# Optimization experiments

Hardware: AMD Instinct MI355X
Metric: run time of the kernel (lower is better)

The kernel has to match this reference:

```python
import jax, jax.numpy as jnp
import numpy as np

B, T, H = 16, 512, 768
S = 32            # gold spans per example
L = 50            # max_span_len -> candidate ends per span
NT = 3            # num_types
HS = 4 * H        # span repr size


def setup_inputs() -> dict:
    key = jax.random.key(0)
    ks = jax.random.split(key, 8)
    h = jax.random.normal(ks[0], (B, T, H), dtype=jnp.float32)
    attention_mask = jnp.ones((B, T), dtype=jnp.int32)
    starts = jax.random.randint(ks[1], (B, S), 1, 400).astype(jnp.int32)
    lens = jax.random.randint(ks[2], (B, S), 0, L).astype(jnp.int32)
    ends = starts + lens                      # <= 448 < last_tok=510
    types = jax.random.randint(ks[3], (B, S), 0, NT).astype(jnp.int32)
    W1 = jax.random.normal(ks[4], (HS, HS), dtype=jnp.float32) * (1.0 / np.sqrt(HS))
    b1 = jnp.zeros((HS,), dtype=jnp.float32)
    w_score = jax.random.normal(ks[5], (HS,), dtype=jnp.float32) * (1.0 / np.sqrt(HS))
    b_score = jnp.zeros((1,), dtype=jnp.float32)
    W_type = jax.random.normal(ks[6], (HS, NT), dtype=jnp.float32) * (1.0 / np.sqrt(HS))
    b_type = jnp.zeros((NT,), dtype=jnp.float32)
    return {"h": h, "attention_mask": attention_mask, "span_starts": starts,
            "span_ends": ends, "span_types": types, "W1": W1, "b1": b1,
            "w_score": w_score, "b_score": b_score, "W_type": W_type, "b_type": b_type}


def _span_loss(h, attention_mask, span_starts, span_ends, span_types,
               W1, b1, w_score, b_score, W_type, b_type, type_loss_weight=1.0):
    cls = h[:, 0]                                              # [B,H]
    # prefix sums for O(1) segment means: pre[b,t] = sum h[b,0:t]
    pre = jnp.concatenate([jnp.zeros((B, 1, H), h.dtype), jnp.cumsum(h, axis=1)], axis=1)

    valid_len = attention_mask.sum(axis=1)                     # [B]
    last_tok = jnp.maximum(1, valid_len - 2)                   # [B]

    s = span_starts                                            # [B,S]
    e_gold = span_ends
    gold_idx = e_gold - s                                      # [B,S]
    lt = last_tok[:, None]
    span_valid = (s >= 1) & (s <= lt) & (e_gold >= s) & (e_gold <= lt) & (gold_idx < L)

    e_max = jnp.minimum(s + L - 1, lt)                         # [B,S]
    p = s[..., None] + jnp.arange(L, dtype=s.dtype)            # [B,S,L] candidate ends
    cand_valid = p <= e_max[..., None]

    sc = jnp.clip(s, 0, T - 1)
    pc = jnp.clip(p, 0, T - 1)
    bi2 = jnp.arange(B)[:, None]
    bi3 = jnp.arange(B)[:, None, None]

    h_start = h[bi2, sc]                                       # [B,S,H]
    h_end = h[bi3, pc]                                         # [B,S,L,H]
    seg_len = jnp.maximum(p - s[..., None] + 1, 1).astype(h.dtype)
    h_mean = (pre[bi3, pc + 1] - pre[bi2, sc][:, :, None]) / seg_len[..., None]

    repr_ = jnp.concatenate([
        jnp.broadcast_to(h_start[:, :, None], (B, S, L, H)),
        h_end,
        h_mean,
        jnp.broadcast_to(cls[:, None, None], (B, S, L, H)),
    ], axis=-1)                                                # [B,S,L,4H]

    h1 = jax.nn.gelu(jnp.einsum('bslh,hd->bsld', repr_, W1) + b1, approximate=False)
    scores = jnp.einsum('bsld,d->bsl', h1, w_score) + b_score[0]      # [B,S,L]
    type_logits = jnp.einsum('bsld,dk->bslk', h1, W_type) + b_type    # [B,S,L,NT]

    # end-index CE over valid candidate ends
    masked = jnp.where(cand_valid, scores, jnp.float32(-1e9))
    logp_end = jax.nn.log_softmax(masked, axis=-1)             # [B,S,L]
    gi = jnp.clip(gold_idx, 0, L - 1)
    end_loss = -jnp.take_along_axis(logp_end, gi[..., None], axis=-1)[..., 0]  # [B,S]

    # type CE at the gold end index
    tl_gold = jnp.take_along_axis(type_logits, gi[..., None, None], axis=2)[:, :, 0]  # [B,S,NT]
    logp_t = jax.nn.log_softmax(tl_gold, axis=-1)
    tg = jnp.clip(span_types, 0, NT - 1)
    type_loss = -jnp.take_along_axis(logp_t, tg[..., None], axis=-1)[..., 0]  # [B,S]

    vmask = span_valid.astype(h.dtype)
    n_seg = vmask.sum()
    denom = jnp.maximum(n_seg, 1.0)
    loss_end = jnp.where(n_seg > 0, (end_loss * vmask).sum() / denom, 0.0)
    loss_type = jnp.where(n_seg > 0, (type_loss * vmask).sum() / denom, 0.0)
    return loss_end + type_loss_weight * loss_type


def reference(h, attention_mask, span_starts, span_ends, span_types,
              W1, b1, w_score, b_score, W_type, b_type):
    return _span_loss(h, attention_mask, span_starts, span_ends, span_types,
                      W1, b1, w_score, b_score, W_type, b_type)
```

## Files before the change

kernel.cpp:

```cpp
#include <hip/hip_runtime.h>
#include <hip/hip_bf16.h>
#include <math.h>

#define B_ 16
#define T_ 512
#define H_ 768
#define S_ 32
#define L_ 50
#define NT_ 3
#define HS_ 3072
#define CH_ 8
#define CT_ 64

#define XROWS 8192
#define YBASE 8192
#define GBASE 16512
#define XYROWS 16400
#define AROWS 17152

typedef __attribute__((ext_vector_type(8))) short short8;
typedef __attribute__((ext_vector_type(4))) float float4v;

__device__ __forceinline__ float bf2f(unsigned short u) {
    union { unsigned int i; float f; } v; v.i = ((unsigned int)u) << 16; return v.f;
}
__device__ __forceinline__ void load_lds16(const void* g, void* l) {
    __builtin_amdgcn_global_load_lds((__attribute__((address_space(1))) void*)g,
                                     (__attribute__((address_space(3))) void*)l, 16, 0, 0);
}

__device__ __forceinline__ float gelu_exact(float v) {
    float a = fabsf(v) * 0.70710678118654752f;
    float t = __builtin_amdgcn_rcpf(fmaf(a, 0.47047f, 1.0f));
    float poly = t * fmaf(t, fmaf(t, 0.7478556f, -0.0958798f), 0.3480242f);
    float e = __builtin_amdgcn_exp2f(a * a * -1.4426950408889634f);
    float erfa = fmaf(-poly, e, 1.0f);
    float erfv = copysignf(erfa, v);
    return 0.5f * v * (1.0f + erfv);
}

__global__ __launch_bounds__(256) void cumsum_pass1(const float* __restrict__ h,
                                                    float* __restrict__ partial) {
    int idx = blockIdx.x * 256 + threadIdx.x;
    int hd = idx % H_; int t = idx / H_; int ch = t % CH_; int b = t / CH_;
    const float* hp = h + ((size_t)b * T_ + ch * CT_) * H_ + hd;
    float acc = 0.f;
#pragma unroll 8
    for (int tt = 0; tt < CT_; tt++) acc += hp[(size_t)tt * H_];
    partial[idx] = acc;
}

__global__ __launch_bounds__(256) void cumsum_pass2(float* __restrict__ partial) {
    int idx = blockIdx.x * 256 + threadIdx.x;
    int hd = idx % H_, b = idx / H_;
    float acc = 0.f;
#pragma unroll
    for (int ch = 0; ch < CH_; ch++) {
        size_t o = ((size_t)b * CH_ + ch) * H_ + hd;
        float v = partial[o];
        partial[o] = acc;
        acc += v;
    }
}

__global__ __launch_bounds__(256) void cumsum_pass3(const float* __restrict__ h,
                                                    const float* __restrict__ partial,
                                                    __hip_bfloat16* __restrict__ Ab) {
    int idx = blockIdx.x * 256 + threadIdx.x;
    int hd = idx % H_; int t = idx / H_; int ch = t % CH_; int b = t / CH_;
    float acc = partial[idx];
    int row0 = b * T_ + ch * CT_;
    const float* hp = h + (size_t)row0 * H_ + hd;
    __hip_bfloat16* hb = Ab + (size_t)row0 * H_ + hd;
    __hip_bfloat16* pp = Ab + ((size_t)(YBASE + b * (T_ + 1) + ch * CT_ + 1)) * H_ + hd;
    if (ch == 0) Ab[((size_t)(YBASE + b * (T_ + 1))) * H_ + hd] = __float2bfloat16(0.f);
#pragma unroll 8
    for (int tt = 0; tt < CT_; tt++) {
        float hv = hp[(size_t)tt * H_];
        hb[(size_t)tt * H_] = __float2bfloat16(hv);
        acc += hv;
        pp[(size_t)tt * H_] = __float2bfloat16(acc);
    }
}

__global__ void gather_kernel(const float* __restrict__ h,
                              const int* __restrict__ starts,
                              __hip_bfloat16* __restrict__ Ab) {
    int r = blockIdx.x;
    int src_row;
    if (r < B_ * S_) {
        int b = r / S_;
        int sv = starts[r];
        int sc = min(max(sv, 0), T_ - 1);
        src_row = b * T_ + sc;
    } else {
        int b = r - B_ * S_;
        src_row = b * T_;
    }
    __hip_bfloat16* dst = Ab + (size_t)(GBASE + r) * H_;
    for (int j = threadIdx.x; j < H_; j += 256)
        dst[j] = __float2bfloat16(h[(size_t)src_row * H_ + j]);
}

__global__ __launch_bounds__(256) void transpose_w(const float* __restrict__ W1,
                                                   __hip_bfloat16* __restrict__ Wt) {
    __shared__ float tile[64][65];
    int n0 = blockIdx.x * 64, k0 = blockIdx.y * 64;
    int c = threadIdx.x & 63, r0 = threadIdx.x >> 6;
#pragma unroll
    for (int i = 0; i < 16; i++) {
        int r = r0 + i * 4;
        tile[r][c] = W1[(size_t)(k0 + r) * HS_ + n0 + c];
    }
    __syncthreads();
    int p = k0 / H_, kl = k0 % H_;
    __hip_bfloat16* out = Wt + (size_t)p * HS_ * H_;
#pragma unroll
    for (int i = 0; i < 16; i++) {
        int r = r0 + i * 4;
        out[(size_t)(n0 + r) * H_ + kl + c] = __float2bfloat16(tile[c][r]);
    }
}

__global__ __launch_bounds__(256) void mfma_gemm(const __hip_bfloat16* __restrict__ Ab,
                                                 const __hip_bfloat16* __restrict__ Wt,
                                                 __hip_bfloat16* __restrict__ XY,
                                                 float* __restrict__ ST,
                                                 float* __restrict__ CC) {
    constexpr int K = H_;
    __shared__ __hip_bfloat16 As[128 * 32];
    __shared__ __hip_bfloat16 Bs[128 * 32];
    int tid = threadIdx.x;
    int wave = tid >> 6, lane = tid & 63;
    int m0 = blockIdx.y * 128, n0 = blockIdx.x * 128;
    int wm = (wave & 1) * 64, wn = (wave >> 1) * 64;

    const __hip_bfloat16* Bt;
    if (m0 < XROWS)            Bt = Wt + (size_t)1 * HS_ * H_;
    else if (m0 < GBASE)       Bt = Wt + (size_t)2 * HS_ * H_;
    else if (m0 < GBASE + 512) Bt = Wt;
    else                       Bt = Wt + (size_t)3 * HS_ * H_;

    float4v acc[4][4] = {};

    int c1 = wave * 128 + lane;
    int c2 = c1 + 64;
    int lr = lane & 15, lq = lane >> 4;

    for (int k0 = 0; k0 < K; k0 += 32) {
        __syncthreads();
        load_lds16(Ab + (size_t)(m0 + (c1 >> 2)) * K + k0 + (c1 & 3) * 8,
                   &As[(size_t)(wave * 128) * 8]);
        load_lds16(Ab + (size_t)(m0 + (c2 >> 2)) * K + k0 + (c2 & 3) * 8,
                   &As[(size_t)(wave * 128 + 64) * 8]);
        load_lds16(Bt + (size_t)(n0 + (c1 >> 2)) * K + k0 + (c1 & 3) * 8,
                   &Bs[(size_t)(wave * 128) * 8]);
        load_lds16(Bt + (size_t)(n0 + (c2 >> 2)) * K + k0 + (c2 & 3) * 8,
                   &Bs[(size_t)(wave * 128 + 64) * 8]);
        __syncthreads();

        short8 af[4], bf[4];
        const short* Asp = (const short*)As;
        const short* Bsp = (const short*)Bs;
#pragma unroll
        for (int mi = 0; mi < 4; mi++)
            af[mi] = *(const short8*)&Asp[(wm + mi * 16 + lr) * 32 + lq * 8];
#pragma unroll
        for (int ni = 0; ni < 4; ni++)
            bf[ni] = *(const short8*)&Bsp[(wn + ni * 16 + lr) * 32 + lq * 8];
#pragma unroll
        for (int mi = 0; mi < 4; mi++)
#pragma unroll
            for (int ni = 0; ni < 4; ni++)
                acc[mi][ni] = __builtin_amdgcn_mfma_f32_16x16x32_bf16(
                    af[mi], bf[ni], acc[mi][ni], 0, 0, 0);
    }

    int col = lane & 15, rq = (lane >> 4) * 4;
#pragma unroll
    for (int mi = 0; mi < 4; mi++) {
#pragma unroll
        for (int ni = 0; ni < 4; ni++) {
#pragma unroll
            for (int r = 0; r < 4; r++) {
                int m = m0 + wm + mi * 16 + rq + r;
                int n = n0 + wn + ni * 16 + col;
                float v = acc[mi][ni][r];
                if (m < XYROWS) {
                    XY[(size_t)m * HS_ + n] = __float2bfloat16(v);
                } else if (m >= GBASE && m < GBASE + 512) {
                    ST[(size_t)(m - GBASE) * HS_ + n] = v;
                } else if (m >= GBASE + 512 && m < GBASE + 528) {
                    CC[(size_t)(m - GBASE - 512) * HS_ + n] = v;
                }
            }
        }
    }
}

__global__ __launch_bounds__(256) void c0_kernel(float4* __restrict__ ST,
                                                 const float4* __restrict__ CC,
                                                 const float4* __restrict__ b1) {
    int i = blockIdx.x * 256 + threadIdx.x;
    int row = i / (HS_ / 4);
    int b = row >> 5;
    int c4 = i % (HS_ / 4);
    float4 s = ST[i], c = CC[b * (HS_ / 4) + c4], bb = b1[c4];
    s.x += c.x + bb.x; s.y += c.y + bb.y; s.z += c.z + bb.z; s.w += c.w + bb.w;
    ST[i] = s;
}

__global__ __launch_bounds__(256) void combine_kernel(
    const float* __restrict__ c0, const __hip_bfloat16* __restrict__ XY,
    const float* __restrict__ w_score, const float* __restrict__ b_score,
    const float* __restrict__ W_type,
    const int* __restrict__ starts, const int* __restrict__ ends,
    float* __restrict__ scores, float* __restrict__ tgold) {
    int bs = blockIdx.x;
    int b = bs >> 5;
    int wave = threadIdx.x >> 6, lane = threadIdx.x & 63;
    int l = blockIdx.y * 4 + wave;
    if (l >= L_) return;
    int sv = starts[bs], ev = ends[bs];
    int gi = min(max(ev - sv, 0), L_ - 1);
    int sc = min(max(sv, 0), T_ - 1);
    int p = sv + l;
    int pc = min(max(p, 0), T_ - 1);
    float invlen = 1.0f / (float)(l + 1);
    bool isg = (l == gi);

    const unsigned short* Xr = (const unsigned short*)(XY + (size_t)(b * T_ + pc) * HS_);
    const unsigned short* Yp = (const unsigned short*)(XY + (size_t)(YBASE + b * (T_ + 1) + pc + 1) * HS_);
    const unsigned short* Ys = (const unsigned short*)(XY + (size_t)(YBASE + b * (T_ + 1) + sc) * HS_);
    const float* c0r = c0 + (size_t)bs * HS_;

    float local = 0.f, t0 = 0.f, t1 = 0.f, t2 = 0.f;
#pragma unroll
    for (int j = 0; j < 6; j++) {
        int d = j * 512 + lane * 8;
        short8 xv = *(const short8*)(Xr + d);
        short8 yv = *(const short8*)(Yp + d);
        short8 sv8 = *(const short8*)(Ys + d);
        float4 ca = *(const float4*)(c0r + d);
        float4 cb = *(const float4*)(c0r + d + 4);
        float4 wa = *(const float4*)(w_score + d);
        float4 wb = *(const float4*)(w_score + d + 4);
        float cv[8] = {ca.x, ca.y, ca.z, ca.w, cb.x, cb.y, cb.z, cb.w};
        float wv[8] = {wa.x, wa.y, wa.z, wa.w, wb.x, wb.y, wb.z, wb.w};
#pragma unroll
        for (int q = 0; q < 8; q++) {
            float x = bf2f(((const unsigned short*)&xv)[q]);
            float y = bf2f(((const unsigned short*)&yv)[q]);
            float ys = bf2f(((const unsigned short*)&sv8)[q]);
            float v = fmaf(y - ys, invlen, cv[q]) + x;
            float g = gelu_exact(v);
            local = fmaf(g, wv[q], local);
            if (isg) {
                t0 = fmaf(g, W_type[(d + q) * NT_ + 0], t0);
                t1 = fmaf(g, W_type[(d + q) * NT_ + 1], t1);
                t2 = fmaf(g, W_type[(d + q) * NT_ + 2], t2);
            }
        }
    }
#pragma unroll
    for (int off = 32; off >= 1; off >>= 1) local += __shfl_down(local, off);
    if (lane == 0) scores[(size_t)bs * L_ + l] = local + b_score[0];
    if (isg) {
#pragma unroll
        for (int off = 32; off >= 1; off >>= 1) {
            t0 += __shfl_down(t0, off);
            t1 += __shfl_down(t1, off);
            t2 += __shfl_down(t2, off);
        }
        if (lane == 0) {
            tgold[bs * NT_ + 0] = t0;
            tgold[bs * NT_ + 1] = t1;
            tgold[bs * NT_ + 2] = t2;
        }
    }
}

__global__ __launch_bounds__(512) void loss_kernel(
    const float* __restrict__ scores, const float* __restrict__ tgold,
    const int* __restrict__ mask, const int* __restrict__ starts,
    const int* __restrict__ ends, const int* __restrict__ types,
    const float* __restrict__ b_type, float* __restrict__ out) {
    __shared__ int svl[B_];
    __shared__ float r[3][8];
    int tid = threadIdx.x;
    int b = tid / S_;
    if (tid < B_) svl[tid] = 0;
    __syncthreads();
    {
        int part = 0;
        const int* mp = mask + tid * 16;
#pragma unroll
        for (int i = 0; i < 16; i++) part += mp[i];
        atomicAdd(&svl[tid / (T_ / 16)], part);
    }
    __syncthreads();
    int vl = svl[b];
    int lt = max(1, vl - 2);
    int sv = starts[tid], ev = ends[tid];
    int gold = ev - sv;
    bool valid = (sv >= 1) && (sv <= lt) && (ev >= sv) && (ev <= lt) && (gold < L_);
    int emax = min(sv + L_ - 1, lt);
    const float* sp = scores + (size_t)tid * L_;
    float m = -1e30f;
    for (int l = 0; l < L_; l++) {
        float v = (sv + l <= emax) ? sp[l] : -1e9f;
        m = fmaxf(m, v);
    }
    float sum = 0.f;
    for (int l = 0; l < L_; l++) {
        float v = (sv + l <= emax) ? sp[l] : -1e9f;
        sum += expf(v - m);
    }
    int gi = min(max(gold, 0), L_ - 1);
    float vg = (sv + gi <= emax) ? sp[gi] : -1e9f;
    float end_loss = (m + logf(sum)) - vg;

    float t0 = tgold[tid * 3 + 0] + b_type[0];
    float t1 = tgold[tid * 3 + 1] + b_type[1];
    float t2 = tgold[tid * 3 + 2] + b_type[2];
    float tm = fmaxf(t0, fmaxf(t1, t2));
    float tsum = expf(t0 - tm) + expf(t1 - tm) + expf(t2 - tm);
    int tg = min(max(types[tid], 0), NT_ - 1);
    float tv = (tg == 0) ? t0 : ((tg == 1) ? t1 : t2);
    float type_loss = (tm + logf(tsum)) - tv;

    float ve = valid ? end_loss : 0.f;
    float vt = valid ? type_loss : 0.f;
    float vc = valid ? 1.f : 0.f;
    for (int off = 32; off >= 1; off >>= 1) {
        ve += __shfl_down(ve, off);
        vt += __shfl_down(vt, off);
        vc += __shfl_down(vc, off);
    }
    if ((tid & 63) == 0) {
        int w = tid >> 6;
        r[0][w] = ve; r[1][w] = vt; r[2][w] = vc;
    }
    __syncthreads();
    if (tid == 0) {
        float se = 0, st = 0, n = 0;
        for (int w = 0; w < 8; w++) { se += r[0][w]; st += r[1][w]; n += r[2][w]; }
        float denom = fmaxf(n, 1.f);
        out[0] = (n > 0.f) ? (se / denom + st / denom) : 0.f;
    }
}

extern "C" void kernel_launch(void* const* d_in, const int* in_sizes, int n_in,
                              void* d_out, int out_size, void* d_ws, size_t ws_size,
                              hipStream_t stream) {
    const float* h       = (const float*)d_in[0];
    const int*   mask    = (const int*)d_in[1];
    const int*   starts  = (const int*)d_in[2];
    const int*   ends    = (const int*)d_in[3];
    const int*   types   = (const int*)d_in[4];
    const float* W1      = (const float*)d_in[5];
    const float* b1      = (const float*)d_in[6];
    const float* w_score = (const float*)d_in[7];
    const float* b_score = (const float*)d_in[8];
    const float* W_type  = (const float*)d_in[9];
    const float* b_type  = (const float*)d_in[10];
    float* out = (float*)d_out;

    char* ws = (char*)d_ws;
    size_t off = 0;
    __hip_bfloat16* Ab = (__hip_bfloat16*)(ws + off); off += (size_t)AROWS * H_ * 2;
    __hip_bfloat16* XY = (__hip_bfloat16*)(ws + off); off += (size_t)XYROWS * HS_ * 2;
    __hip_bfloat16* Wt = (__hip_bfloat16*)(ws + off); off += (size_t)4 * HS_ * H_ * 2;
    float* ST     = (float*)(ws + off);               off += (size_t)512 * HS_ * 4;
    float* CC     = (float*)(ws + off);               off += (size_t)16 * HS_ * 4;
    float* scores = (float*)(ws + off);               off += (size_t)B_ * S_ * L_ * 4;
    float* tgold  = (float*)(ws + off);               off += (size_t)B_ * S_ * NT_ * 4;
    float* partial = (float*)XY;

    hipLaunchKernelGGL(cumsum_pass1, dim3(B_ * CH_ * H_ / 256), dim3(256), 0, stream, h, partial);
    hipLaunchKernelGGL(cumsum_pass2, dim3(B_ * H_ / 256), dim3(256), 0, stream, partial);
    hipLaunchKernelGGL(cumsum_pass3, dim3(B_ * CH_ * H_ / 256), dim3(256), 0, stream, h, partial, Ab);
    hipLaunchKernelGGL(gather_kernel, dim3(B_ * S_ + B_), dim3(256), 0, stream, h, starts, Ab);
    hipLaunchKernelGGL(transpose_w, dim3(48, 48), dim3(256), 0, stream, W1, Wt);

    hipLaunchKernelGGL(mfma_gemm, dim3(24, AROWS / 128), dim3(256), 0, stream,
                       Ab, Wt, XY, ST, CC);
    hipLaunchKernelGGL(c0_kernel, dim3(512 * HS_ / 4 / 256), dim3(256), 0, stream,
                       (float4*)ST, (const float4*)CC, (const float4*)b1);
    hipLaunchKernelGGL(combine_kernel, dim3(B_ * S_, 13), dim3(256), 0, stream,
                       ST, XY, w_score, b_score, W_type, starts, ends, scores, tgold);
    hipLaunchKernelGGL(loss_kernel, dim3(1), dim3(512), 0, stream,
                       scores, tgold, mask, starts, ends, types, b_type, out);
}
```

Before: 376.0 us.

## Switch GEMM to 32x32 MFMA with K=64 steps, fuse scan pass, bf16 c0

```diff
diff --git a/kernel.cpp b/kernel.cpp
--- a/kernel.cpp
+++ b/kernel.cpp
@@ -19,8 +19,12 @@
 #define AROWS 17152
 
 typedef __attribute__((ext_vector_type(8))) short short8;
-typedef __attribute__((ext_vector_type(4))) float float4v;
-
+typedef __attribute__((ext_vector_type(16))) float float16v;
+
+__device__ __forceinline__ unsigned short f2bf(float f) {
+    __hip_bfloat16 b = __float2bfloat16(f);
+    return *(unsigned short*)&b;
+}
 __device__ __forceinline__ float bf2f(unsigned short u) {
     union { unsigned int i; float f; } v; v.i = ((unsigned int)u) << 16; return v.f;
 }
@@ -50,25 +54,15 @@
     partial[idx] = acc;
 }
 
-__global__ __launch_bounds__(256) void cumsum_pass2(float* __restrict__ partial) {
-    int idx = blockIdx.x * 256 + threadIdx.x;
-    int hd = idx % H_, b = idx / H_;
-    float acc = 0.f;
-#pragma unroll
-    for (int ch = 0; ch < CH_; ch++) {
-        size_t o = ((size_t)b * CH_ + ch) * H_ + hd;
-        float v = partial[o];
-        partial[o] = acc;
-        acc += v;
-    }
-}
-
 __global__ __launch_bounds__(256) void cumsum_pass3(const float* __restrict__ h,
                                                     const float* __restrict__ partial,
                                                     __hip_bfloat16* __restrict__ Ab) {
     int idx = blockIdx.x * 256 + threadIdx.x;
     int hd = idx % H_; int t = idx / H_; int ch = t % CH_; int b = t / CH_;
-    float acc = partial[idx];
+    float acc = 0.f;
+#pragma unroll
+    for (int c = 0; c < CH_; c++)
+        if (c < ch) acc += partial[((size_t)b * CH_ + c) * H_ + hd];
     int row0 = b * T_ + ch * CT_;
     const float* hp = h + (size_t)row0 * H_ + hd;
     __hip_bfloat16* hb = Ab + (size_t)row0 * H_ + hd;
@@ -128,11 +122,11 @@
                                                  float* __restrict__ ST,
                                                  float* __restrict__ CC) {
     constexpr int K = H_;
-    __shared__ __hip_bfloat16 As[128 * 32];
-    __shared__ __hip_bfloat16 Bs[128 * 32];
+    __shared__ __hip_bfloat16 As[2][128][32];
+    __shared__ __hip_bfloat16 Bs[2][128][32];
     int tid = threadIdx.x;
     int wave = tid >> 6, lane = tid & 63;
-    int m0 = blockIdx.y * 128, n0 = blockIdx.x * 128;
+    int m0 = blockIdx.x * 128, n0 = blockIdx.y * 128;
     int wm = (wave & 1) * 64, wn = (wave >> 1) * 64;
 
     const __hip_bfloat16* Bt;
@@ -141,50 +135,54 @@
     else if (m0 < GBASE + 512) Bt = Wt;
     else                       Bt = Wt + (size_t)3 * HS_ * H_;
 
-    float4v acc[4][4] = {};
-
-    int c1 = wave * 128 + lane;
-    int c2 = c1 + 64;
-    int lr = lane & 15, lq = lane >> 4;
-
-    for (int k0 = 0; k0 < K; k0 += 32) {
+    float16v acc[2][2] = {};
+
+    int l31 = lane & 31, lh = lane >> 5;
+
+    for (int k0 = 0; k0 < K; k0 += 64) {
         __syncthreads();
-        load_lds16(Ab + (size_t)(m0 + (c1 >> 2)) * K + k0 + (c1 & 3) * 8,
-                   &As[(size_t)(wave * 128) * 8]);
-        load_lds16(Ab + (size_t)(m0 + (c2 >> 2)) * K + k0 + (c2 & 3) * 8,
-                   &As[(size_t)(wave * 128 + 64) * 8]);
-        load_lds16(Bt + (size_t)(n0 + (c1 >> 2)) * K + k0 + (c1 & 3) * 8,
-                   &Bs[(size_t)(wave * 128) * 8]);
-        load_lds16(Bt + (size_t)(n0 + (c2 >> 2)) * K + k0 + (c2 & 3) * 8,
-                   &Bs[(size_t)(wave * 128 + 64) * 8]);
+#pragma unroll
+        for (int i = 0; i < 4; i++) {
+            int c = i * 256 + wave * 64 + lane;
+            int hh = c >> 9, row = (c >> 2) & 127, kc = c & 3;
+            size_t go = (size_t)row * K + k0 + hh * 32 + kc * 8;
+            char* ldsbase = (char*)As + (size_t)(i * 256 + wave * 64) * 16;
+            load_lds16(Ab + (size_t)m0 * K + go, ldsbase);
+            char* ldsbaseB = (char*)Bs + (size_t)(i * 256 + wave * 64) * 16;
+            load_lds16(Bt + (size_t)n0 * K + go, ldsbaseB);
+        }
         __syncthreads();
 
-        short8 af[4], bf[4];
         const short* Asp = (const short*)As;
         const short* Bsp = (const short*)Bs;
 #pragma unroll
-        for (int mi = 0; mi < 4; mi++)
-            af[mi] = *(const short8*)&Asp[(wm + mi * 16 + lr) * 32 + lq * 8];
-#pragma unroll
-        for (int ni = 0; ni < 4; ni++)
-            bf[ni] = *(const short8*)&Bsp[(wn + ni * 16 + lr) * 32 + lq * 8];
-#pragma unroll
-        for (int mi = 0; mi < 4; mi++)
-#pragma unroll
-            for (int ni = 0; ni < 4; ni++)
-                acc[mi][ni] = __builtin_amdgcn_mfma_f32_16x16x32_bf16(
-                    af[mi], bf[ni], acc[mi][ni], 0, 0, 0);
-    }
-
-    int col = lane & 15, rq = (lane >> 4) * 4;
-#pragma unroll
-    for (int mi = 0; mi < 4; mi++) {
-#pragma unroll
-        for (int ni = 0; ni < 4; ni++) {
-#pragma unroll
-            for (int r = 0; r < 4; r++) {
-                int m = m0 + wm + mi * 16 + rq + r;
-                int n = n0 + wn + ni * 16 + col;
+        for (int kk = 0; kk < 4; kk++) {
+            int hh = kk >> 1;
+            int ko = (kk & 1) * 16 + lh * 8;
+            short8 af[2], bf[2];
+#pragma unroll
+            for (int mi = 0; mi < 2; mi++)
+                af[mi] = *(const short8*)&Asp[hh * 4096 + (wm + mi * 32 + l31) * 32 + ko];
+#pragma unroll
+            for (int ni = 0; ni < 2; ni++)
+                bf[ni] = *(const short8*)&Bsp[hh * 4096 + (wn + ni * 32 + l31) * 32 + ko];
+#pragma unroll
+            for (int mi = 0; mi < 2; mi++)
+#pragma unroll
+                for (int ni = 0; ni < 2; ni++)
+                    acc[mi][ni] = __builtin_amdgcn_mfma_f32_32x32x16_bf16(
+                        af[mi], bf[ni], acc[mi][ni], 0, 0, 0);
+        }
+    }
+
+#pragma unroll
+    for (int mi = 0; mi < 2; mi++) {
+#pragma unroll
+        for (int ni = 0; ni < 2; ni++) {
+            int n = n0 + wn + ni * 32 + l31;
+#pragma unroll
+            for (int r = 0; r < 16; r++) {
+                int m = m0 + wm + mi * 32 + (r & 3) + 8 * (r >> 2) + 4 * lh;
                 float v = acc[mi][ni][r];
                 if (m < XYROWS) {
                     XY[(size_t)m * HS_ + n] = __float2bfloat16(v);
@@ -198,20 +196,25 @@
     }
 }
 
-__global__ __launch_bounds__(256) void c0_kernel(float4* __restrict__ ST,
+__global__ __launch_bounds__(256) void c0_kernel(const float4* __restrict__ ST,
                                                  const float4* __restrict__ CC,
-                                                 const float4* __restrict__ b1) {
+                                                 const float4* __restrict__ b1,
+                                                 ushort4* __restrict__ c0b) {
     int i = blockIdx.x * 256 + threadIdx.x;
     int row = i / (HS_ / 4);
     int b = row >> 5;
     int c4 = i % (HS_ / 4);
     float4 s = ST[i], c = CC[b * (HS_ / 4) + c4], bb = b1[c4];
-    s.x += c.x + bb.x; s.y += c.y + bb.y; s.z += c.z + bb.z; s.w += c.w + bb.w;
-    ST[i] = s;
+    ushort4 o;
+    o.x = f2bf(s.x + c.x + bb.x);
+    o.y = f2bf(s.y + c.y + bb.y);
+    o.z = f2bf(s.z + c.z + bb.z);
+    o.w = f2bf(s.w + c.w + bb.w);
+    c0b[i] = o;
 }
 
 __global__ __launch_bounds__(256) void combine_kernel(
-    const float* __restrict__ c0, const __hip_bfloat16* __restrict__ XY,
+    const unsigned short* __restrict__ c0, const __hip_bfloat16* __restrict__ XY,
     const float* __restrict__ w_score, const float* __restrict__ b_score,
     const float* __restrict__ W_type,
     const int* __restrict__ starts, const int* __restrict__ ends,
@@ -232,7 +235,7 @@
     const unsigned short* Xr = (const unsigned short*)(XY + (size_t)(b * T_ + pc) * HS_);
     const unsigned short* Yp = (const unsigned short*)(XY + (size_t)(YBASE + b * (T_ + 1) + pc + 1) * HS_);
     const unsigned short* Ys = (const unsigned short*)(XY + (size_t)(YBASE + b * (T_ + 1) + sc) * HS_);
-    const float* c0r = c0 + (size_t)bs * HS_;
+    const unsigned short* c0r = c0 + (size_t)bs * HS_;
 
     float local = 0.f, t0 = 0.f, t1 = 0.f, t2 = 0.f;
 #pragma unroll
@@ -241,18 +244,17 @@
         short8 xv = *(const short8*)(Xr + d);
         short8 yv = *(const short8*)(Yp + d);
         short8 sv8 = *(const short8*)(Ys + d);
-        float4 ca = *(const float4*)(c0r + d);
-        float4 cb = *(const float4*)(c0r + d + 4);
+        short8 cv8 = *(const short8*)(c0r + d);
         float4 wa = *(const float4*)(w_score + d);
         float4 wb = *(const float4*)(w_score + d + 4);
-        float cv[8] = {ca.x, ca.y, ca.z, ca.w, cb.x, cb.y, cb.z, cb.w};
         float wv[8] = {wa.x, wa.y, wa.z, wa.w, wb.x, wb.y, wb.z, wb.w};
 #pragma unroll
         for (int q = 0; q < 8; q++) {
             float x = bf2f(((const unsigned short*)&xv)[q]);
             float y = bf2f(((const unsigned short*)&yv)[q]);
             float ys = bf2f(((const unsigned short*)&sv8)[q]);
-            float v = fmaf(y - ys, invlen, cv[q]) + x;
+            float cv = bf2f(((const unsigned short*)&cv8)[q]);
+            float v = fmaf(y - ys, invlen, cv) + x;
             float g = gelu_exact(v);
             local = fmaf(g, wv[q], local);
             if (isg) {
@@ -373,22 +375,23 @@
     __hip_bfloat16* Wt = (__hip_bfloat16*)(ws + off); off += (size_t)4 * HS_ * H_ * 2;
     float* ST     = (float*)(ws + off);               off += (size_t)512 * HS_ * 4;
     float* CC     = (float*)(ws + off);               off += (size_t)16 * HS_ * 4;
+    unsigned short* c0b = (unsigned short*)(ws + off); off += (size_t)512 * HS_ * 2;
     float* scores = (float*)(ws + off);               off += (size_t)B_ * S_ * L_ * 4;
     float* tgold  = (float*)(ws + off);               off += (size_t)B_ * S_ * NT_ * 4;
     float* partial = (float*)XY;
 
     hipLaunchKernelGGL(cumsum_pass1, dim3(B_ * CH_ * H_ / 256), dim3(256), 0, stream, h, partial);
-    hipLaunchKernelGGL(cumsum_pass2, dim3(B_ * H_ / 256), dim3(256), 0, stream, partial);
     hipLaunchKernelGGL(cumsum_pass3, dim3(B_ * CH_ * H_ / 256), dim3(256), 0, stream, h, partial, Ab);
     hipLaunchKernelGGL(gather_kernel, dim3(B_ * S_ + B_), dim3(256), 0, stream, h, starts, Ab);
     hipLaunchKernelGGL(transpose_w, dim3(48, 48), dim3(256), 0, stream, W1, Wt);
 
-    hipLaunchKernelGGL(mfma_gemm, dim3(24, AROWS / 128), dim3(256), 0, stream,
+    hipLaunchKernelGGL(mfma_gemm, dim3(AROWS / 128, 24), dim3(256), 0, stream,
                        Ab, Wt, XY, ST, CC);
     hipLaunchKernelGGL(c0_kernel, dim3(512 * HS_ / 4 / 256), dim3(256), 0, stream,
-                       (float4*)ST, (const float4*)CC, (const float4*)b1);
+                       (const float4*)ST, (const float4*)CC, (const float4*)b1,
+                       (ushort4*)c0b);
     hipLaunchKernelGGL(combine_kernel, dim3(B_ * S_, 13), dim3(256), 0, stream,
-                       ST, XY, w_score, b_score, W_type, starts, ends, scores, tgold);
+                       c0b, XY, w_score, b_score, W_type, starts, ends, scores, tgold);
     hipLaunchKernelGGL(loss_kernel, dim3(1), dim3(512), 0, stream,
                        scores, tgold, mask, starts, ends, types, b_type, out);
 }
```

Measured after the change: 364.5 us. 1.03x faster.
